# Performance work log

Measured on AMD Instinct MI355X. Metric: run time of the kernel, lower is better.

## Reference

```python
import jax, jax.numpy as jnp
import numpy as np
from jax import lax

H = 1024
E = 8
TOP_K = 2


def setup_inputs() -> dict:
    key = jax.random.key(0)
    kx, k1, k2 = jax.random.split(key, 3)
    x = jax.random.normal(kx, (8, 2048, H), dtype=jnp.float32)
    # router MLP params, init normal(0, 0.02), zero bias (matches _init_weights)
    w1 = jax.random.normal(k1, (H, 2 * H), dtype=jnp.float32) * 0.02
    b1 = jnp.zeros((2 * H,), dtype=jnp.float32)
    w2 = jax.random.normal(k2, (2 * H, E), dtype=jnp.float32) * 0.02
    b2 = jnp.zeros((E,), dtype=jnp.float32)
    return {"x": x, "w1": w1, "b1": b1, "w2": w2, "b2": b2}


def reference(x, w1, b1, w2, b2):
    # gating MLP: Linear -> GELU (exact, torch default) -> Linear
    h = jax.nn.gelu(jnp.einsum('bsh,hf->bsf', x, w1) + b1, approximate=False)
    expert_weights = jnp.einsum('bsf,fe->bse', h, w2) + b2  # [B,S,E]

    top_k_weights, top_k_indices = lax.top_k(expert_weights, TOP_K)  # [B,S,K]
    top_k_weights = jax.nn.softmax(top_k_weights, axis=-1)

    # scatter renormalized weights into dense [B,S,E] mask (indices distinct -> one-hot sum)
    onehot = jax.nn.one_hot(top_k_indices, E, dtype=expert_weights.dtype)  # [B,S,K,E]
    masks = jnp.einsum('bsk,bske->bse', top_k_weights, onehot)

    expert_usage = masks.sum(axis=(0, 1))
    expert_usage = expert_usage / expert_usage.sum()
    target_usage = jnp.full_like(expert_usage, 1.0 / E)
    load_balancing_loss = jnp.mean((expert_usage - target_usage) ** 2)

    sparsity_loss = jnp.mean(jnp.sum(masks > 0, axis=-1).astype(jnp.float32)) / TOP_K
    total_loss = load_balancing_loss + 0.1 * sparsity_loss

    return expert_weights, masks, total_loss, expert_usage
```

## Files before the change

kernel.cpp:

```cpp
#include <hip/hip_runtime.h>
#include <math.h>

#define HDIM 1024
#define FDIM 2048
#define NEXP 8
#define MTOK 16384
#define NSLC 32
#define BM 128
#define BN 128

typedef __attribute__((ext_vector_type(8))) short bf16x8;
typedef __attribute__((ext_vector_type(4))) float f32x4;

__device__ inline unsigned short f2bf_rne(float f) {
    unsigned int u = __float_as_uint(f);
    u = (u + 0x7FFFu + ((u >> 16) & 1u)) >> 16;
    return (unsigned short)u;
}
__device__ inline float bf2f(unsigned short h) {
    unsigned int u = ((unsigned int)h) << 16;
    return __uint_as_float(u);
}

__global__ __launch_bounds__(256) void cvt_x(const float* __restrict__ x,
                                             unsigned short* __restrict__ af)
{
    __shared__ unsigned short hs[16384];
    __shared__ unsigned short ls[16384];
    const int mt = blockIdx.x;
    const float* src = x + (size_t)mt * 16384;
    const int m = threadIdx.x & 15;
    const int kseg = threadIdx.x >> 4;

    #pragma unroll
    for (int c = 0; c < 8; c++) {
        int k = c * 128 + kseg * 8;
        float v[8];
        *(float4*)(v)     = *(const float4*)(src + m * 1024 + k);
        *(float4*)(v + 4) = *(const float4*)(src + m * 1024 + k + 4);
        union { unsigned short u[8]; uint4 q; } oh, ol;
        #pragma unroll
        for (int j = 0; j < 8; j++) {
            unsigned short h = f2bf_rne(v[j]);
            oh.u[j] = h;
            ol.u[j] = f2bf_rne(v[j] - bf2f(h));
        }
        int kb = k >> 5, q = (k >> 3) & 3;
        int o = kb * 512 + m * 32 + q * 8;
        *(uint4*)(hs + o) = oh.q;
        *(uint4*)(ls + o) = ol.q;
    }
    __syncthreads();
    unsigned short* dst = af + (size_t)mt * 32768;
    #pragma unroll
    for (int c = 0; c < 16; c++) {
        int f = c * 2048 + threadIdx.x * 8;
        int kb = f >> 10, half = (f >> 9) & 1, idx = f & 511;
        int q = idx >> 7, mm = (idx >> 3) & 15;
        const unsigned short* s = (half ? ls : hs) + kb * 512 + mm * 32 + q * 8;
        *(uint4*)(dst + f) = *(const uint4*)s;
    }
}

__global__ __launch_bounds__(256) void cvt_w1f(const float* __restrict__ w1,
                                               unsigned short* __restrict__ wf)
{
    __shared__ float t[32][33];
    int n0 = blockIdx.x * 32;
    int k0 = blockIdx.y * 32;
    int lx = threadIdx.x & 31, ly = threadIdx.x >> 5;
    #pragma unroll
    for (int r = 0; r < 32; r += 8)
        t[ly + r][lx] = w1[(size_t)(k0 + ly + r) * FDIM + n0 + lx];
    __syncthreads();
    #pragma unroll
    for (int r = 0; r < 32; r += 8) {
        float v = t[lx][ly + r];
        unsigned short h = f2bf_rne(v);
        unsigned short l = f2bf_rne(v - bf2f(h));
        int n = n0 + ly + r, k = k0 + lx;
        size_t base = (size_t)((n >> 4) * 32 + (k >> 5)) * 1024;
        int lj = (((k >> 3) & 3) * 16 + (n & 15)) * 8 + (k & 7);
        wf[base + lj] = h;
        wf[base + 512 + lj] = l;
    }
}

__global__ __launch_bounds__(256, 2) void gemm1_mfma(
    const unsigned short* __restrict__ af, const unsigned short* __restrict__ wf,
    const float* __restrict__ b1, const float* __restrict__ w2,
    float* __restrict__ part)
{
    const int tid  = threadIdx.x;
    const int lane = tid & 63;
    const int l15  = lane & 15;
    const int q    = lane >> 4;
    const int wave = tid >> 6;
    const int wm   = wave & 1;
    const int wn   = wave >> 1;

    const int id = blockIdx.x;
    const int xcd = id & 7, seq = id >> 3;
    const int strip = seq >> 6;
    const int bn = (seq >> 2) & 15;
    const int bmo = seq & 3;
    const int bm = strip * 32 + xcd * 4 + bmo;
    const int m0 = bm * BM, n0 = bn * BN;

    const unsigned short* apt[4];
    const unsigned short* bpt[4];
    #pragma unroll
    for (int i = 0; i < 4; i++) {
        apt[i] = af + ((size_t)(bm * 8 + wm * 4 + i) * 32) * 1024 + lane * 8;
        bpt[i] = wf + ((size_t)(bn * 8 + wn * 4 + i) * 32) * 1024 + lane * 8;
    }

    f32x4 acc[4][4];
    #pragma unroll
    for (int i = 0; i < 4; i++)
        #pragma unroll
        for (int j = 0; j < 4; j++) acc[i][j] = (f32x4){0.f, 0.f, 0.f, 0.f};

    bf16x8 Ah0[4], Al0[4], Bh0[4], Bl0[4];
    bf16x8 Ah1[4], Al1[4], Bh1[4], Bl1[4];

    #pragma unroll
    for (int i = 0; i < 4; i++) {
        Ah0[i] = *(const bf16x8*)(apt[i]);
        Al0[i] = *(const bf16x8*)(apt[i] + 512);
        Bh0[i] = *(const bf16x8*)(bpt[i]);
        Bl0[i] = *(const bf16x8*)(bpt[i] + 512);
    }

    #pragma unroll 1
    for (int t = 0; t < 32; t += 2) {
        #pragma unroll
        for (int i = 0; i < 4; i++) {
            Ah1[i] = *(const bf16x8*)(apt[i] + 1024);
            Al1[i] = *(const bf16x8*)(apt[i] + 1536);
            Bh1[i] = *(const bf16x8*)(bpt[i] + 1024);
            Bl1[i] = *(const bf16x8*)(bpt[i] + 1536);
        }
        #pragma unroll
        for (int i = 0; i < 4; i++)
            #pragma unroll
            for (int j = 0; j < 4; j++) {
                acc[i][j] = __builtin_amdgcn_mfma_f32_16x16x32_bf16(
                    Ah0[i], Bh0[j], acc[i][j], 0, 0, 0);
                acc[i][j] = __builtin_amdgcn_mfma_f32_16x16x32_bf16(
                    Ah0[i], Bl0[j], acc[i][j], 0, 0, 0);
                acc[i][j] = __builtin_amdgcn_mfma_f32_16x16x32_bf16(
                    Al0[i], Bh0[j], acc[i][j], 0, 0, 0);
            }
        #pragma unroll
        for (int i = 0; i < 4; i++) { apt[i] += 2048; bpt[i] += 2048; }
        if (t + 2 < 32) {
            #pragma unroll
            for (int i = 0; i < 4; i++) {
                Ah0[i] = *(const bf16x8*)(apt[i]);
                Al0[i] = *(const bf16x8*)(apt[i] + 512);
                Bh0[i] = *(const bf16x8*)(bpt[i]);
                Bl0[i] = *(const bf16x8*)(bpt[i] + 512);
            }
        }
        #pragma unroll
        for (int i = 0; i < 4; i++)
            #pragma unroll
            for (int j = 0; j < 4; j++) {
                acc[i][j] = __builtin_amdgcn_mfma_f32_16x16x32_bf16(
                    Ah1[i], Bh1[j], acc[i][j], 0, 0, 0);
                acc[i][j] = __builtin_amdgcn_mfma_f32_16x16x32_bf16(
                    Ah1[i], Bl1[j], acc[i][j], 0, 0, 0);
                acc[i][j] = __builtin_amdgcn_mfma_f32_16x16x32_bf16(
                    Al1[i], Bh1[j], acc[i][j], 0, 0, 0);
            }
    }

    #pragma unroll
    for (int j = 0; j < 4; j++) {
        int n = n0 + wn * 64 + j * 16 + l15;
        float bb = b1[n];
        #pragma unroll
        for (int i = 0; i < 4; i++)
            #pragma unroll
            for (int r = 0; r < 4; r++) {
                float v = acc[i][j][r] + bb;
                acc[i][j][r] = 0.5f * v * (1.0f + erff(v * 0.70710678118654752f));
            }
    }

    float w2r[4][8];
    #pragma unroll
    for (int j = 0; j < 4; j++) {
        const float4* p = (const float4*)(w2 + (size_t)(n0 + wn * 64 + j * 16 + l15) * NEXP);
        float4 u = p[0], v = p[1];
        w2r[j][0] = u.x; w2r[j][1] = u.y; w2r[j][2] = u.z; w2r[j][3] = u.w;
        w2r[j][4] = v.x; w2r[j][5] = v.y; w2r[j][6] = v.z; w2r[j][7] = v.w;
    }

    const int sl = bn * 2 + wn;
    #pragma unroll
    for (int e = 0; e < NEXP; e++) {
        float p[4][4];
        #pragma unroll
        for (int i = 0; i < 4; i++)
            #pragma unroll
            for (int r = 0; r < 4; r++) {
                float s = 0.f;
                #pragma unroll
                for (int j = 0; j < 4; j++) s += acc[i][j][r] * w2r[j][e];
                p[i][r] = s;
            }
        #pragma unroll
        for (int off = 1; off < 16; off <<= 1)
            #pragma unroll
            for (int i = 0; i < 4; i++)
                #pragma unroll
                for (int r = 0; r < 4; r++)
                    p[i][r] += __shfl_xor(p[i][r], off);
        if (l15 == 0) {
            #pragma unroll
            for (int i = 0; i < 4; i++)
                #pragma unroll
                for (int r = 0; r < 4; r++) {
                    int m = m0 + wm * 64 + i * 16 + q * 4 + r;
                    part[(size_t)sl * (MTOK * NEXP) + (size_t)m * NEXP + e] = p[i][r];
                }
        }
    }
}

__global__ __launch_bounds__(256) void router_topk(
    const float* __restrict__ part, const float* __restrict__ b2,
    float* __restrict__ out, float* __restrict__ gu, int* __restrict__ gc)
{
    const int t = blockIdx.x * 256 + threadIdx.x;

    float logit[8];
    #pragma unroll
    for (int e = 0; e < 8; e++) logit[e] = b2[e];
    #pragma unroll
    for (int j = 0; j < NSLC; j++) {
        const float4* p4 = (const float4*)(part + (size_t)j * (MTOK * NEXP) + (size_t)t * NEXP);
        float4 u = p4[0], v = p4[1];
        logit[0] += u.x; logit[1] += u.y; logit[2] += u.z; logit[3] += u.w;
        logit[4] += v.x; logit[5] += v.y; logit[6] += v.z; logit[7] += v.w;
    }

    int i1 = 0; float v1 = logit[0];
    #pragma unroll
    for (int e = 1; e < 8; e++) { if (logit[e] > v1) { v1 = logit[e]; i1 = e; } }
    int i2 = -1; float v2 = -INFINITY;
    #pragma unroll
    for (int e = 0; e < 8; e++) {
        if (e != i1 && logit[e] > v2) { v2 = logit[e]; i2 = e; }
    }
    float ex = expf(v2 - v1);
    float inv = 1.0f / (1.0f + ex);
    float wa = inv, wb = ex * inv;

    float4* o = (float4*)(out + (size_t)t * NEXP);
    o[0] = make_float4(logit[0], logit[1], logit[2], logit[3]);
    o[1] = make_float4(logit[4], logit[5], logit[6], logit[7]);

    float mk[8];
    #pragma unroll
    for (int e = 0; e < 8; e++) mk[e] = 0.0f;
    mk[i1] = wa; mk[i2] = wb;
    float4* om = (float4*)(out + (size_t)(MTOK * NEXP) + (size_t)t * NEXP);
    om[0] = make_float4(mk[0], mk[1], mk[2], mk[3]);
    om[1] = make_float4(mk[4], mk[5], mk[6], mk[7]);

    __shared__ float us[8];
    __shared__ int cs;
    if (threadIdx.x < 8) us[threadIdx.x] = 0.0f;
    if (threadIdx.x == 0) cs = 0;
    __syncthreads();
    atomicAdd(&us[i1], wa);
    atomicAdd(&us[i2], wb);
    int cnt = (wa > 0.0f ? 1 : 0) + (wb > 0.0f ? 1 : 0);
    atomicAdd(&cs, cnt);
    __syncthreads();
    if (threadIdx.x < 8) atomicAdd(&gu[threadIdx.x], us[threadIdx.x]);
    if (threadIdx.x == 0) atomicAdd(gc, cs);
}

__global__ void router_final(const float* __restrict__ gu, const int* __restrict__ gc,
                             float* __restrict__ out)
{
    if (blockIdx.x == 0 && threadIdx.x == 0) {
        float u[8]; float tot = 0.0f;
        for (int e = 0; e < 8; e++) { u[e] = gu[e]; tot += u[e]; }
        float lb = 0.0f;
        for (int e = 0; e < 8; e++) {
            float un = u[e] / tot;
            out[2 * MTOK * NEXP + 1 + e] = un;
            float d = un - 0.125f;
            lb += d * d;
        }
        lb *= (1.0f / 8.0f);
        float sp = ((float)(*gc) / (float)MTOK) * 0.5f;
        out[2 * MTOK * NEXP] = lb + 0.1f * sp;
    }
}

extern "C" void kernel_launch(void* const* d_in, const int* in_sizes, int n_in,
                              void* d_out, int out_size, void* d_ws, size_t ws_size,
                              hipStream_t stream) {
    const float* x  = (const float*)d_in[0];
    const float* w1 = (const float*)d_in[1];
    const float* b1 = (const float*)d_in[2];
    const float* w2 = (const float*)d_in[3];
    const float* b2 = (const float*)d_in[4];
    float* out = (float*)d_out;

    unsigned short* af = (unsigned short*)d_ws;
    unsigned short* wf = af + (size_t)1024 * 32768;
    float* part = (float*)(wf + (size_t)128 * 32 * 1024);
    float* gu = part + (size_t)NSLC * MTOK * NEXP;
    int* gc = (int*)(gu + 8);

    hipMemsetAsync(gu, 0, 64, stream);

    cvt_x<<<1024, 256, 0, stream>>>(x, af);
    cvt_w1f<<<dim3(FDIM / 32, HDIM / 32), 256, 0, stream>>>(w1, wf);
    gemm1_mfma<<<2048, 256, 0, stream>>>(af, wf, b1, w2, part);
    router_topk<<<MTOK / 256, 256, 0, stream>>>(part, b2, out, gu, gc);
    router_final<<<1, 64, 0, stream>>>(gu, gc, out);
}
```

Measured before the change: 345.8 us.

## Switch GEMM to 32x32x16 MFMA with 256x128 block tiles

Replaces the 16x16x32 bf16 MFMA with the 32x32x16 variant and repacks the pre-converted x and w1 buffers into 32-row, 16-k fragments to match. Block tiles grow from 128x128 to 256x128 and the grid shrinks to 1024 blocks. The goal is higher MFMA throughput per instruction and fewer operand loads per flop. The epilogue reduction now uses 32-lane shuffles over 64 accumulators per tile, which raises register pressure and shuffle work.

```diff
diff --git a/kernel.cpp b/kernel.cpp
--- a/kernel.cpp
+++ b/kernel.cpp
@@ -6,11 +6,10 @@
 #define NEXP 8
 #define MTOK 16384
 #define NSLC 32
-#define BM 128
-#define BN 128
+
 
 typedef __attribute__((ext_vector_type(8))) short bf16x8;
-typedef __attribute__((ext_vector_type(4))) float f32x4;
+typedef __attribute__((ext_vector_type(16))) float f32x16;
 
 __device__ inline unsigned short f2bf_rne(float f) {
     unsigned int u = __float_as_uint(f);
@@ -28,37 +27,43 @@
     __shared__ unsigned short hs[16384];
     __shared__ unsigned short ls[16384];
     const int mt = blockIdx.x;
-    const float* src = x + (size_t)mt * 16384;
-    const int m = threadIdx.x & 15;
-    const int kseg = threadIdx.x >> 4;
-
-    #pragma unroll
-    for (int c = 0; c < 8; c++) {
-        int k = c * 128 + kseg * 8;
-        float v[8];
-        *(float4*)(v)     = *(const float4*)(src + m * 1024 + k);
-        *(float4*)(v + 4) = *(const float4*)(src + m * 1024 + k + 4);
-        union { unsigned short u[8]; uint4 q; } oh, ol;
-        #pragma unroll
-        for (int j = 0; j < 8; j++) {
-            unsigned short h = f2bf_rne(v[j]);
-            oh.u[j] = h;
-            ol.u[j] = f2bf_rne(v[j] - bf2f(h));
-        }
-        int kb = k >> 5, q = (k >> 3) & 3;
-        int o = kb * 512 + m * 32 + q * 8;
-        *(uint4*)(hs + o) = oh.q;
-        *(uint4*)(ls + o) = ol.q;
-    }
-    __syncthreads();
-    unsigned short* dst = af + (size_t)mt * 32768;
-    #pragma unroll
-    for (int c = 0; c < 16; c++) {
-        int f = c * 2048 + threadIdx.x * 8;
-        int kb = f >> 10, half = (f >> 9) & 1, idx = f & 511;
-        int q = idx >> 7, mm = (idx >> 3) & 15;
-        const unsigned short* s = (half ? ls : hs) + kb * 512 + mm * 32 + q * 8;
-        *(uint4*)(dst + f) = *(const uint4*)s;
+    const int m = threadIdx.x & 31;
+    const int kc = threadIdx.x >> 5;
+    const float* src = x + ((size_t)mt * 32 + m) * HDIM;
+    unsigned short* dst = af + (size_t)mt * 65536;
+
+    #pragma unroll
+    for (int p = 0; p < 2; p++) {
+        #pragma unroll
+        for (int i = 0; i < 8; i++) {
+            int k_local = kc * 64 + i * 8;
+            int k = p * 512 + k_local;
+            float v[8];
+            *(float4*)(v)     = *(const float4*)(src + k);
+            *(float4*)(v + 4) = *(const float4*)(src + k + 4);
+            union { unsigned short u[8]; uint4 q; } oh, ol;
+            #pragma unroll
+            for (int j = 0; j < 8; j++) {
+                unsigned short h = f2bf_rne(v[j]);
+                oh.u[j] = h;
+                ol.u[j] = f2bf_rne(v[j] - bf2f(h));
+            }
+            int ks_l = k_local >> 4;
+            int lane = ((k_local >> 3) & 1) * 32 + m;
+            int o = ks_l * 512 + lane * 8;
+            *(uint4*)(hs + o) = oh.q;
+            *(uint4*)(ls + o) = ol.q;
+        }
+        __syncthreads();
+        unsigned short* dp = dst + p * 32768;
+        #pragma unroll
+        for (int c = 0; c < 16; c++) {
+            int f = c * 2048 + threadIdx.x * 8;
+            int ks_l = f >> 10, hl = (f >> 9) & 1, rest = f & 511;
+            const unsigned short* s = (hl ? ls : hs) + ks_l * 512 + rest;
+            *(uint4*)(dp + f) = *(const uint4*)s;
+        }
+        __syncthreads();
     }
 }
 
@@ -79,8 +84,8 @@
         unsigned short h = f2bf_rne(v);
         unsigned short l = f2bf_rne(v - bf2f(h));
         int n = n0 + ly + r, k = k0 + lx;
-        size_t base = (size_t)((n >> 4) * 32 + (k >> 5)) * 1024;
-        int lj = (((k >> 3) & 3) * 16 + (n & 15)) * 8 + (k & 7);
+        size_t base = ((size_t)(n >> 5) * 64 + (k >> 4)) * 1024;
+        int lj = (((k >> 3) & 1) * 32 + (n & 31)) * 8 + (k & 7);
         wf[base + lj] = h;
         wf[base + 512 + lj] = l;
     }
@@ -93,106 +98,120 @@
 {
     const int tid  = threadIdx.x;
     const int lane = tid & 63;
-    const int l15  = lane & 15;
-    const int q    = lane >> 4;
+    const int l31  = lane & 31;
+    const int half = lane >> 5;
     const int wave = tid >> 6;
     const int wm   = wave & 1;
     const int wn   = wave >> 1;
 
     const int id = blockIdx.x;
     const int xcd = id & 7, seq = id >> 3;
-    const int strip = seq >> 6;
-    const int bn = (seq >> 2) & 15;
-    const int bmo = seq & 3;
-    const int bm = strip * 32 + xcd * 4 + bmo;
-    const int m0 = bm * BM, n0 = bn * BN;
-
-    const unsigned short* apt[4];
-    const unsigned short* bpt[4];
+    const int strip = seq >> 5;
+    const int bn = (seq >> 1) & 15;
+    const int bmo = seq & 1;
+    const int bm = strip * 16 + xcd * 2 + bmo;
+    const int m0 = bm * 256, n0 = bn * 128;
+
+    const unsigned short* ap[4];
+    const unsigned short* bp[2];
+    #pragma unroll
+    for (int i = 0; i < 4; i++)
+        ap[i] = af + (size_t)(bm * 8 + wm * 4 + i) * 65536 + lane * 8;
+    #pragma unroll
+    for (int j = 0; j < 2; j++)
+        bp[j] = wf + (size_t)(bn * 4 + wn * 2 + j) * 65536 + lane * 8;
+
+    f32x16 acc[4][2];
+    #pragma unroll
+    for (int i = 0; i < 4; i++)
+        #pragma unroll
+        for (int j = 0; j < 2; j++)
+            #pragma unroll
+            for (int r = 0; r < 16; r++) acc[i][j][r] = 0.f;
+
+    bf16x8 Ah0[4], Al0[4], Bh0[2], Bl0[2];
+    bf16x8 Ah1[4], Al1[4], Bh1[2], Bl1[2];
+
     #pragma unroll
     for (int i = 0; i < 4; i++) {
-        apt[i] = af + ((size_t)(bm * 8 + wm * 4 + i) * 32) * 1024 + lane * 8;
-        bpt[i] = wf + ((size_t)(bn * 8 + wn * 4 + i) * 32) * 1024 + lane * 8;
-    }
-
-    f32x4 acc[4][4];
-    #pragma unroll
-    for (int i = 0; i < 4; i++)
-        #pragma unroll
-        for (int j = 0; j < 4; j++) acc[i][j] = (f32x4){0.f, 0.f, 0.f, 0.f};
-
-    bf16x8 Ah0[4], Al0[4], Bh0[4], Bl0[4];
-    bf16x8 Ah1[4], Al1[4], Bh1[4], Bl1[4];
-
-    #pragma unroll
-    for (int i = 0; i < 4; i++) {
-        Ah0[i] = *(const bf16x8*)(apt[i]);
-        Al0[i] = *(const bf16x8*)(apt[i] + 512);
-        Bh0[i] = *(const bf16x8*)(bpt[i]);
-        Bl0[i] = *(const bf16x8*)(bpt[i] + 512);
+        Ah0[i] = *(const bf16x8*)(ap[i]);
+        Al0[i] = *(const bf16x8*)(ap[i] + 512);
+    }
+    #pragma unroll
+    for (int j = 0; j < 2; j++) {
+        Bh0[j] = *(const bf16x8*)(bp[j]);
+        Bl0[j] = *(const bf16x8*)(bp[j] + 512);
     }
 
     #pragma unroll 1
-    for (int t = 0; t < 32; t += 2) {
+    for (int t = 0; t < 64; t += 2) {
         #pragma unroll
         for (int i = 0; i < 4; i++) {
-            Ah1[i] = *(const bf16x8*)(apt[i] + 1024);
-            Al1[i] = *(const bf16x8*)(apt[i] + 1536);
-            Bh1[i] = *(const bf16x8*)(bpt[i] + 1024);
-            Bl1[i] = *(const bf16x8*)(bpt[i] + 1536);
+            Ah1[i] = *(const bf16x8*)(ap[i] + 1024);
+            Al1[i] = *(const bf16x8*)(ap[i] + 1536);
+        }
+        #pragma unroll
+        for (int j = 0; j < 2; j++) {
+            Bh1[j] = *(const bf16x8*)(bp[j] + 1024);
+            Bl1[j] = *(const bf16x8*)(bp[j] + 1536);
         }
         #pragma unroll
         for (int i = 0; i < 4; i++)
             #pragma unroll
-            for (int j = 0; j < 4; j++) {
-                acc[i][j] = __builtin_amdgcn_mfma_f32_16x16x32_bf16(
+            for (int j = 0; j < 2; j++) {
+                acc[i][j] = __builtin_amdgcn_mfma_f32_32x32x16_bf16(
                     Ah0[i], Bh0[j], acc[i][j], 0, 0, 0);
-                acc[i][j] = __builtin_amdgcn_mfma_f32_16x16x32_bf16(
+                acc[i][j] = __builtin_amdgcn_mfma_f32_32x32x16_bf16(
                     Ah0[i], Bl0[j], acc[i][j], 0, 0, 0);
-                acc[i][j] = __builtin_amdgcn_mfma_f32_16x16x32_bf16(
+                acc[i][j] = __builtin_amdgcn_mfma_f32_32x32x16_bf16(
                     Al0[i], Bh0[j], acc[i][j], 0, 0, 0);
             }
         #pragma unroll
-        for (int i = 0; i < 4; i++) { apt[i] += 2048; bpt[i] += 2048; }
-        if (t + 2 < 32) {
+        for (int i = 0; i < 4; i++) ap[i] += 2048;
+        #pragma unroll
+        for (int j = 0; j < 2; j++) bp[j] += 2048;
+        if (t + 2 < 64) {
             #pragma unroll
             for (int i = 0; i < 4; i++) {
-                Ah0[i] = *(const bf16x8*)(apt[i]);
-                Al0[i] = *(const bf16x8*)(apt[i] + 512);
-                Bh0[i] = *(const bf16x8*)(bpt[i]);
-                Bl0[i] = *(const bf16x8*)(bpt[i] + 512);
+                Ah0[i] = *(const bf16x8*)(ap[i]);
+                Al0[i] = *(const bf16x8*)(ap[i] + 512);
+            }
+            #pragma unroll
+            for (int j = 0; j < 2; j++) {
+                Bh0[j] = *(const bf16x8*)(bp[j]);
+                Bl0[j] = *(const bf16x8*)(bp[j] + 512);
             }
         }
         #pragma unroll
         for (int i = 0; i < 4; i++)
             #pragma unroll
-            for (int j = 0; j < 4; j++) {
-                acc[i][j] = __builtin_amdgcn_mfma_f32_16x16x32_bf16(
+            for (int j = 0; j < 2; j++) {
+                acc[i][j] = __builtin_amdgcn_mfma_f32_32x32x16_bf16(
                     Ah1[i], Bh1[j], acc[i][j], 0, 0, 0);
-                acc[i][j] = __builtin_amdgcn_mfma_f32_16x16x32_bf16(
+                acc[i][j] = __builtin_amdgcn_mfma_f32_32x32x16_bf16(
                     Ah1[i], Bl1[j], acc[i][j], 0, 0, 0);
-                acc[i][j] = __builtin_amdgcn_mfma_f32_16x16x32_bf16(
+                acc[i][j] = __builtin_amdgcn_mfma_f32_32x32x16_bf16(
                     Al1[i], Bh1[j], acc[i][j], 0, 0, 0);
             }
     }
 
     #pragma unroll
-    for (int j = 0; j < 4; j++) {
-        int n = n0 + wn * 64 + j * 16 + l15;
+    for (int j = 0; j < 2; j++) {
+        int n = n0 + wn * 64 + j * 32 + l31;
         float bb = b1[n];
         #pragma unroll
         for (int i = 0; i < 4; i++)
             #pragma unroll
-            for (int r = 0; r < 4; r++) {
+            for (int r = 0; r < 16; r++) {
                 float v = acc[i][j][r] + bb;
                 acc[i][j][r] = 0.5f * v * (1.0f + erff(v * 0.70710678118654752f));
             }
     }
 
-    float w2r[4][8];
-    #pragma unroll
-    for (int j = 0; j < 4; j++) {
-        const float4* p = (const float4*)(w2 + (size_t)(n0 + wn * 64 + j * 16 + l15) * NEXP);
+    float w2r[2][8];
+    #pragma unroll
+    for (int j = 0; j < 2; j++) {
+        const float4* p = (const float4*)(w2 + (size_t)(n0 + wn * 64 + j * 32 + l31) * NEXP);
         float4 u = p[0], v = p[1];
         w2r[j][0] = u.x; w2r[j][1] = u.y; w2r[j][2] = u.z; w2r[j][3] = u.w;
         w2r[j][4] = v.x; w2r[j][5] = v.y; w2r[j][6] = v.z; w2r[j][7] = v.w;
@@ -201,29 +220,25 @@
     const int sl = bn * 2 + wn;
     #pragma unroll
     for (int e = 0; e < NEXP; e++) {
-        float p[4][4];
+        float p[4][16];
         #pragma unroll
         for (int i = 0; i < 4; i++)
             #pragma unroll
-            for (int r = 0; r < 4; r++) {
-                float s = 0.f;
-                #pragma unroll
-                for (int j = 0; j < 4; j++) s += acc[i][j][r] * w2r[j][e];
-                p[i][r] = s;
-            }
-        #pragma unroll
-        for (int off = 1; off < 16; off <<= 1)
+            for (int r = 0; r < 16; r++)
+                p[i][r] = acc[i][0][r] * w2r[0][e] + acc[i][1][r] * w2r[1][e];
+        #pragma unroll
+        for (int off = 1; off < 32; off <<= 1)
             #pragma unroll
             for (int i = 0; i < 4; i++)
                 #pragma unroll
-                for (int r = 0; r < 4; r++)
+                for (int r = 0; r < 16; r++)
                     p[i][r] += __shfl_xor(p[i][r], off);
-        if (l15 == 0) {
+        if (l31 == 0) {
             #pragma unroll
             for (int i = 0; i < 4; i++)
                 #pragma unroll
-                for (int r = 0; r < 4; r++) {
-                    int m = m0 + wm * 64 + i * 16 + q * 4 + r;
+                for (int r = 0; r < 16; r++) {
+                    int m = m0 + wm * 128 + i * 32 + (r & 3) + 8 * (r >> 2) + 4 * half;
                     part[(size_t)sl * (MTOK * NEXP) + (size_t)m * NEXP + e] = p[i][r];
                 }
         }
@@ -315,16 +330,16 @@
     float* out = (float*)d_out;
 
     unsigned short* af = (unsigned short*)d_ws;
-    unsigned short* wf = af + (size_t)1024 * 32768;
-    float* part = (float*)(wf + (size_t)128 * 32 * 1024);
+    unsigned short* wf = af + (size_t)512 * 65536;
+    float* part = (float*)(wf + (size_t)64 * 65536);
     float* gu = part + (size_t)NSLC * MTOK * NEXP;
     int* gc = (int*)(gu + 8);
 
     hipMemsetAsync(gu, 0, 64, stream);
 
-    cvt_x<<<1024, 256, 0, stream>>>(x, af);
+    cvt_x<<<512, 256, 0, stream>>>(x, af);
     cvt_w1f<<<dim3(FDIM / 32, HDIM / 32), 256, 0, stream>>>(w1, wf);
-    gemm1_mfma<<<2048, 256, 0, stream>>>(af, wf, b1, w2, part);
+    gemm1_mfma<<<1024, 256, 0, stream>>>(af, wf, b1, w2, part);
     router_topk<<<MTOK / 256, 256, 0, stream>>>(part, b2, out, gu, gc);
     router_final<<<1, 64, 0, stream>>>(gu, gc, out);
 }
```

After: 802.8 us. 2.32x slower.
